# Kernel optimization log

Hardware: AMD Instinct MI355X
Metric: run time of the kernel (lower is better)

The kernel has to match this reference:

```python
import jax, jax.numpy as jnp
import numpy as np

N, K, D_IN, D_OUT = 50000, 16, 256, 256
LN_EPS = 1e-5


def setup_inputs() -> dict:
    key = jax.random.key(0)
    k1, k2, k3, k4 = jax.random.split(key, 4)
    features = jax.random.normal(k1, (N, D_IN), dtype=jnp.float32)
    neighbors = jax.random.randint(k2, (N, K), 0, N, dtype=jnp.int64)
    importance_weights = jax.random.uniform(k3, (N, K), dtype=jnp.float32)
    # Linear(in_channels, out_channels): weight stored as [D_IN, D_OUT] for x @ W + b
    W = jax.random.normal(k4, (D_IN, D_OUT), dtype=jnp.float32) * (1.0 / np.sqrt(D_IN))
    b = jnp.zeros((D_OUT,), dtype=jnp.float32)
    gamma = jnp.ones((D_OUT,), dtype=jnp.float32)
    beta = jnp.zeros((D_OUT,), dtype=jnp.float32)
    return {"features": features, "neighbors": neighbors,
            "importance_weights": importance_weights,
            "W": W, "b": b, "gamma": gamma, "beta": beta}


def reference(features, neighbors, importance_weights, W, b, gamma, beta):
    # Gather neighbor features: [N, K, D_IN]
    neigh_feats = features[neighbors]
    # Linear transform: [N, K, D_OUT]
    transformed = jnp.einsum('nkd,df->nkf', neigh_feats, W) + b
    # Normalize importance weights per node; zero-sum fallback = uniform mean
    wsum = jnp.sum(importance_weights, axis=-1, keepdims=True)  # [N, 1]
    norm_w = jnp.where(wsum == 0.0,
                       jnp.full_like(importance_weights, 1.0 / K),
                       importance_weights / jnp.where(wsum == 0.0, 1.0, wsum))
    # Importance-weighted sum over neighbors: [N, D_OUT]
    agg = jnp.einsum('nkf,nk->nf', transformed, norm_w)
    # LayerNorm over feature dim (torch: biased variance, eps=1e-5)
    mean = jnp.mean(agg, axis=-1, keepdims=True)
    var = jnp.mean((agg - mean) ** 2, axis=-1, keepdims=True)
    out = (agg - mean) * jax.lax.rsqrt(var + LN_EPS) * gamma + beta
    return out
```

## Files before the change

### kernel.cpp

```cpp
#include <hip/hip_runtime.h>


#define NN   50000
#define KNB  16
#define D    256
#define WSTR 272

typedef __attribute__((ext_vector_type(8))) short short8;
typedef __attribute__((ext_vector_type(4))) float f32x4;

static __device__ __forceinline__ unsigned short f2bf(float x) {
    unsigned int u = __float_as_uint(x);
    return (unsigned short)((u + 0x7FFFu + ((u >> 16) & 1u)) >> 16);
}
static __device__ __forceinline__ float bf2f(unsigned short h) {
    return __uint_as_float((unsigned int)h << 16);
}

__global__ __launch_bounds__(256) void convert_all(const float* __restrict__ feat,
                                                   const float* __restrict__ Wm,
                                                   unsigned short* __restrict__ featb,
                                                   unsigned short* __restrict__ wtp,
                                                   int nfb) {
    if ((int)blockIdx.x < nfb) {
        const size_t g = (size_t)blockIdx.x * 256 + threadIdx.x;
        const float4 a = *(const float4*)(feat + g * 8);
        const float4 b = *(const float4*)(feat + g * 8 + 4);
        short8 o;
        o[0] = (short)f2bf(a.x); o[1] = (short)f2bf(a.y);
        o[2] = (short)f2bf(a.z); o[3] = (short)f2bf(a.w);
        o[4] = (short)f2bf(b.x); o[5] = (short)f2bf(b.y);
        o[6] = (short)f2bf(b.z); o[7] = (short)f2bf(b.w);
        *(short8*)(featb + g * 8) = o;
    } else {
        const int g    = (blockIdx.x - nfb) * 256 + threadIdx.x;
        const int lane = g & 63;
        const int c    = (g >> 6) & 15;
        const int kb   = g >> 10;
        const int n    = c * 16 + (lane & 15);
        const int k0   = kb * 32 + (lane >> 4) * 8;
        short8 v;
        #pragma unroll
        for (int j = 0; j < 8; ++j) v[j] = (short)f2bf(Wm[(size_t)(k0 + j) * D + n]);
        *(short8*)(wtp + (size_t)g * 8) = v;
    }
}

__global__ __launch_bounds__(256, 8) void pool_b(const unsigned short* __restrict__ featb,
                                                 const int*   __restrict__ nbr,
                                                 const float* __restrict__ iw,
                                                 unsigned short* __restrict__ aggb) {
    const int  t    = threadIdx.x;
    const int  lane = t & 63;
    const int  wq   = t >> 6;
    const long n    = (long)blockIdx.x * 4 + wq;

    float ws = 0.f;
    #pragma unroll
    for (int k = 0; k < KNB; ++k) ws += iw[n * KNB + k];
    const bool  zs  = (ws == 0.f);
    const float inv = zs ? (1.f / KNB) : (1.f / ws);

    float4 p = make_float4(0.f, 0.f, 0.f, 0.f);
    #pragma unroll 1
    for (int kb = 0; kb < KNB; kb += 8) {
        int   idx[8];
        float w[8];
        #pragma unroll
        for (int k = 0; k < 8; ++k) {
            idx[k] = nbr[n * KNB + kb + k];
            w[k]   = iw [n * KNB + kb + k];
        }
        #pragma unroll
        for (int k = 0; k < 8; ++k) {
            const float   wk = zs ? inv : (w[k] * inv);
            const ushort4 u  = *(const ushort4*)(featb + (size_t)idx[k] * D + lane * 4);
            p.x += wk * bf2f(u.x); p.y += wk * bf2f(u.y);
            p.z += wk * bf2f(u.z); p.w += wk * bf2f(u.w);
        }
    }
    ushort4 o;
    o.x = f2bf(p.x); o.y = f2bf(p.y); o.z = f2bf(p.z); o.w = f2bf(p.w);
    *(ushort4*)(aggb + (size_t)n * 512 + lane * 4) = o;
}

__global__ __launch_bounds__(256, 8) void pool_f(const float* __restrict__ feat,
                                                 const int*   __restrict__ nbr,
                                                 const float* __restrict__ iw,
                                                 unsigned short* __restrict__ aggb) {
    const int  t    = threadIdx.x;
    const int  lane = t & 63;
    const int  wq   = t >> 6;
    const long n    = (long)blockIdx.x * 4 + wq;
    float ws = 0.f;
    #pragma unroll
    for (int k = 0; k < KNB; ++k) ws += iw[n * KNB + k];
    const bool  zs  = (ws == 0.f);
    const float inv = zs ? (1.f / KNB) : (1.f / ws);
    float4 p = make_float4(0.f, 0.f, 0.f, 0.f);
    #pragma unroll 1
    for (int kb = 0; kb < KNB; kb += 8) {
        int idx[8]; float w[8];
        #pragma unroll
        for (int k = 0; k < 8; ++k) { idx[k] = nbr[n*KNB+kb+k]; w[k] = iw[n*KNB+kb+k]; }
        #pragma unroll
        for (int k = 0; k < 8; ++k) {
            const float  wk = zs ? inv : (w[k] * inv);
            const float4 f  = *(const float4*)(feat + (size_t)idx[k] * D + lane * 4);
            p.x += wk*f.x; p.y += wk*f.y; p.z += wk*f.z; p.w += wk*f.w;
        }
    }
    ushort4 o;
    o.x = f2bf(p.x); o.y = f2bf(p.y); o.z = f2bf(p.z); o.w = f2bf(p.w);
    *(ushort4*)(aggb + (size_t)n * 512 + lane * 4) = o;
}

__global__ __launch_bounds__(256) void gemm_ln(const unsigned short* __restrict__ aggb,
                                               const unsigned short* __restrict__ wtp,
                                               const float* __restrict__ bias,
                                               const float* __restrict__ gamma,
                                               const float* __restrict__ beta,
                                               float* __restrict__ out) {
    __shared__ short sB[2][8192];
    __shared__ float fsh[4][4 * WSTR];

    const int t       = threadIdx.x;
    const int lane    = t & 63;
    const int wq      = t >> 6;
    const int quad    = lane >> 4;
    const int l15     = lane & 15;
    const int rowbase = blockIdx.x * 64 + wq * 16;

    const int arow = min(rowbase + l15, NN - 1);
    const unsigned short* aptr = aggb + (size_t)arow * 512 + quad * 8;
    const short8* wv = (const short8*)wtp;

    short8 aF[8];
    #pragma unroll
    for (int kb = 0; kb < 8; ++kb) aF[kb] = *(const short8*)(aptr + kb * 32);

    #pragma unroll
    for (int i = 0; i < 4; ++i)
        *(short8*)&sB[0][(size_t)(i * 256 + t) * 8] = wv[i * 256 + t];
    __syncthreads();

    f32x4 acc[16];
    #pragma unroll
    for (int c = 0; c < 16; ++c) acc[c] = (f32x4){0.f, 0.f, 0.f, 0.f};

    #pragma unroll
    for (int kb = 0; kb < 8; ++kb) {
        const int buf = kb & 1;
        short8 stg[4];
        if (kb < 7) {
            #pragma unroll
            for (int i = 0; i < 4; ++i)
                stg[i] = wv[(size_t)(kb + 1) * 1024 + i * 256 + t];
        }
        #pragma unroll
        for (int c = 0; c < 16; ++c) {
            const short8 b = *(const short8*)&sB[buf][(size_t)(c * 64 + lane) * 8];
            acc[c] = __builtin_amdgcn_mfma_f32_16x16x32_bf16(aF[kb], b, acc[c], 0, 0, 0);
        }
        if (kb < 7) {
            #pragma unroll
            for (int i = 0; i < 4; ++i)
                *(short8*)&sB[buf ^ 1][(size_t)(i * 256 + t) * 8] = stg[i];
        }
        __syncthreads();
    }

    float bv[16];
    #pragma unroll
    for (int c = 0; c < 16; ++c) bv[c] = bias[c * 16 + l15];
    const float4 gv4 = *(const float4*)(gamma + lane * 4);
    const float4 bt4 = *(const float4*)(beta  + lane * 4);
    float* wsh = fsh[wq];

    #pragma unroll
    for (int j = 0; j < 4; ++j) {
        float s = 0.f, sq = 0.f;
        #pragma unroll
        for (int c = 0; c < 16; ++c) {
            const float v = acc[c][j] + bv[c];
            s += v; sq += v * v;
        }
        #pragma unroll
        for (int off = 1; off < 16; off <<= 1) {
            s  += __shfl_xor(s,  off, 64);
            sq += __shfl_xor(sq, off, 64);
        }
        const float mean = s * (1.f / D);
        const float var  = sq * (1.f / D) - mean * mean;
        const float rstd = rsqrtf(var + 1e-5f);
        #pragma unroll
        for (int c = 0; c < 16; ++c)
            wsh[quad * WSTR + c * 16 + l15] = (acc[c][j] + bv[c] - mean) * rstd;
        #pragma unroll
        for (int p = 0; p < 4; ++p) {
            const long  r  = rowbase + p * 4 + j;
            if (r < NN) {
                const float4 v = *(const float4*)(wsh + p * WSTR + lane * 4);
                float4 o;
                o.x = v.x * gv4.x + bt4.x; o.y = v.y * gv4.y + bt4.y;
                o.z = v.z * gv4.z + bt4.z; o.w = v.w * gv4.w + bt4.w;
                *(float4*)(out + r * D + lane * 4) = o;
            }
        }
    }
}

extern "C" void kernel_launch(void* const* d_in, const int* in_sizes, int n_in,
                              void* d_out, int out_size, void* d_ws, size_t ws_size,
                              hipStream_t stream) {
    const float* feat = (const float*)d_in[0];
    const int*   nbr  = (const int*)d_in[1];
    const float* iw   = (const float*)d_in[2];
    const float* Wm   = (const float*)d_in[3];
    const float* b    = (const float*)d_in[4];
    const float* g    = (const float*)d_in[5];
    const float* be   = (const float*)d_in[6];
    float*       out  = (float*)d_out;

    unsigned short* wtp   = (unsigned short*)d_ws;
    unsigned short* featb = (unsigned short*)((char*)d_ws + 131072);
    unsigned short* aggb  = (unsigned short*)d_out;

    const size_t need = 131072 + (size_t)NN * D * 2;

    if (ws_size >= need) {
        convert_all<<<dim3(6282),   dim3(256), 0, stream>>>(feat, Wm, featb, wtp, 6250);
        pool_b     <<<dim3(NN / 4), dim3(256), 0, stream>>>(featb, nbr, iw, aggb);
    } else {
        convert_all<<<dim3(32),     dim3(256), 0, stream>>>(feat, Wm, featb, wtp, 0);
        pool_f     <<<dim3(NN / 4), dim3(256), 0, stream>>>(feat, nbr, iw, aggb);
    }
    gemm_ln<<<dim3((NN + 63) / 64), dim3(256), 0, stream>>>(aggb, wtp, b, g, be, out);
}
```

Before: 186.5 us.

## Split pooling into feature-dimension slices with neighbor-parallel lanes and shuffle reduction

Replaces the per-node pooling kernel with one where each block handles one 32-wide feature slice for 32 nodes. Within a wave, 8 lane groups each gather a different pair of neighbors, and the partial sums are combined with cross-lane shuffles. The slicing is meant to keep each block's gathers within a narrow column band for better cache locality, and to raise memory-level parallelism per node. Index and weight loads and the output store use nontemporal hints. In exchange, it adds shuffle-reduction work, each gather is only 8 bytes per lane, and every neighbor index is re-read once per slice.

```diff
diff --git a/kernel.cpp b/kernel.cpp
--- a/kernel.cpp
+++ b/kernel.cpp
@@ -5,9 +5,11 @@
 #define KNB  16
 #define D    256
 #define WSTR 272
+#define NPB  32
 
 typedef __attribute__((ext_vector_type(8))) short short8;
 typedef __attribute__((ext_vector_type(4))) float f32x4;
+typedef __attribute__((ext_vector_type(4))) unsigned short us4;
 
 static __device__ __forceinline__ unsigned short f2bf(float x) {
     unsigned int u = __float_as_uint(x);
@@ -46,42 +48,59 @@
     }
 }
 
-__global__ __launch_bounds__(256, 8) void pool_b(const unsigned short* __restrict__ featb,
-                                                 const int*   __restrict__ nbr,
-                                                 const float* __restrict__ iw,
-                                                 unsigned short* __restrict__ aggb) {
-    const int  t    = threadIdx.x;
-    const int  lane = t & 63;
-    const int  wq   = t >> 6;
-    const long n    = (long)blockIdx.x * 4 + wq;
-
-    float ws = 0.f;
-    #pragma unroll
-    for (int k = 0; k < KNB; ++k) ws += iw[n * KNB + k];
-    const bool  zs  = (ws == 0.f);
-    const float inv = zs ? (1.f / KNB) : (1.f / ws);
-
-    float4 p = make_float4(0.f, 0.f, 0.f, 0.f);
+__global__ __launch_bounds__(256, 8) void pool_slices(
+        const unsigned short* __restrict__ featb,
+        const int*   __restrict__ nbr,
+        const float* __restrict__ iw,
+        unsigned short* __restrict__ aggb) {
+    const int t     = threadIdx.x;
+    const int lane  = t & 63;
+    const int wq    = t >> 6;
+    const int s     = blockIdx.x & 7;
+    const int chunk = blockIdx.x >> 3;
+    const int dl    = lane & 7;
+    const int kg    = lane >> 3;
+    const int dbase = s * 32 + dl * 4;
+
+    const int n0 = chunk * NPB + wq * (NPB / 4);
     #pragma unroll 1
-    for (int kb = 0; kb < KNB; kb += 8) {
-        int   idx[8];
-        float w[8];
-        #pragma unroll
-        for (int k = 0; k < 8; ++k) {
-            idx[k] = nbr[n * KNB + kb + k];
-            w[k]   = iw [n * KNB + kb + k];
-        }
-        #pragma unroll
-        for (int k = 0; k < 8; ++k) {
-            const float   wk = zs ? inv : (w[k] * inv);
-            const ushort4 u  = *(const ushort4*)(featb + (size_t)idx[k] * D + lane * 4);
-            p.x += wk * bf2f(u.x); p.y += wk * bf2f(u.y);
-            p.z += wk * bf2f(u.z); p.w += wk * bf2f(u.w);
-        }
-    }
-    ushort4 o;
-    o.x = f2bf(p.x); o.y = f2bf(p.y); o.z = f2bf(p.z); o.w = f2bf(p.w);
-    *(ushort4*)(aggb + (size_t)n * 512 + lane * 4) = o;
+    for (int j = 0; j < NPB / 4; ++j) {
+        const int n = n0 + j;
+        if (n >= NN) break;
+        const size_t base = (size_t)n * KNB;
+        const int   i0 = __builtin_nontemporal_load(nbr + base + kg);
+        const int   i1 = __builtin_nontemporal_load(nbr + base + 8 + kg);
+        const float w0 = __builtin_nontemporal_load(iw  + base + kg);
+        const float w1 = __builtin_nontemporal_load(iw  + base + 8 + kg);
+        float ws = w0 + w1;
+        ws += __shfl_xor(ws, 8,  64);
+        ws += __shfl_xor(ws, 16, 64);
+        ws += __shfl_xor(ws, 32, 64);
+        const bool  zsum = (ws == 0.f);
+        const float inv  = zsum ? (1.f / KNB) : (1.f / ws);
+        const float f0   = zsum ? inv : (w0 * inv);
+        const float f1   = zsum ? inv : (w1 * inv);
+        const us4 u0 = *(const us4*)(featb + (size_t)i0 * D + dbase);
+        const us4 u1 = *(const us4*)(featb + (size_t)i1 * D + dbase);
+        float4 p;
+        p.x = f0 * bf2f(u0[0]) + f1 * bf2f(u1[0]);
+        p.y = f0 * bf2f(u0[1]) + f1 * bf2f(u1[1]);
+        p.z = f0 * bf2f(u0[2]) + f1 * bf2f(u1[2]);
+        p.w = f0 * bf2f(u0[3]) + f1 * bf2f(u1[3]);
+        #pragma unroll
+        for (int off = 8; off < 64; off <<= 1) {
+            p.x += __shfl_xor(p.x, off, 64);
+            p.y += __shfl_xor(p.y, off, 64);
+            p.z += __shfl_xor(p.z, off, 64);
+            p.w += __shfl_xor(p.w, off, 64);
+        }
+        if (kg == 0) {
+            us4 o;
+            o[0] = f2bf(p.x); o[1] = f2bf(p.y); o[2] = f2bf(p.z); o[3] = f2bf(p.w);
+            __builtin_nontemporal_store(o,
+                (us4*)(aggb + (size_t)n * 512 + dbase));
+        }
+    }
 }
 
 __global__ __launch_bounds__(256, 8) void pool_f(const float* __restrict__ feat,
@@ -229,10 +248,11 @@
     const size_t need = 131072 + (size_t)NN * D * 2;
 
     if (ws_size >= need) {
-        convert_all<<<dim3(6282),   dim3(256), 0, stream>>>(feat, Wm, featb, wtp, 6250);
-        pool_b     <<<dim3(NN / 4), dim3(256), 0, stream>>>(featb, nbr, iw, aggb);
+        convert_all<<<dim3(6282), dim3(256), 0, stream>>>(feat, Wm, featb, wtp, 6250);
+        pool_slices<<<dim3(8 * ((NN + NPB - 1) / NPB)), dim3(256), 0, stream>>>(
+            featb, nbr, iw, aggb);
     } else {
-        convert_all<<<dim3(32),     dim3(256), 0, stream>>>(feat, Wm, featb, wtp, 0);
+        convert_all<<<dim3(32),   dim3(256), 0, stream>>>(feat, Wm, aggb, wtp, 0);
         pool_f     <<<dim3(NN / 4), dim3(256), 0, stream>>>(feat, nbr, iw, aggb);
     }
     gemm_ln<<<dim3((NN + 63) / 64), dim3(256), 0, stream>>>(aggb, wtp, b, g, be, out);
```

Result: slower. 233.4 us (+25.2%).

## Store bf16 features slice-major and gather per 32-column slice for cache locality

Applied to the files above, without the earlier changes.

The bf16 conversion now writes features in a slice-major layout, with 8 slices of 32 columns each. A new pool kernel assigns each block one slice and 32 nodes, so the random neighbor gathers only touch a 3.2MB slice that can stay resident in L2/LLC. Neighbor indices and weights are loaded cooperatively and broadcast with shuffles, and the aggregate goes to a separate workspace buffer with a 256-element stride. The cost is smaller 8-byte gathers per lane, an extra workspace requirement, and the risk that falling back to the old path changes behaviour when the workspace is too small.

```diff
diff --git a/kernel.cpp b/kernel.cpp
--- a/kernel.cpp
+++ b/kernel.cpp
@@ -8,6 +8,9 @@
 
 typedef __attribute__((ext_vector_type(8))) short short8;
 typedef __attribute__((ext_vector_type(4))) float f32x4;
+typedef __attribute__((ext_vector_type(4))) unsigned short us4;
+typedef __attribute__((ext_vector_type(2))) int   i32x2;
+typedef __attribute__((ext_vector_type(2))) float f32x2;
 
 static __device__ __forceinline__ unsigned short f2bf(float x) {
     unsigned int u = __float_as_uint(x);
@@ -21,7 +24,7 @@
                                                    const float* __restrict__ Wm,
                                                    unsigned short* __restrict__ featb,
                                                    unsigned short* __restrict__ wtp,
-                                                   int nfb) {
+                                                   int nfb, int slicemaj) {
     if ((int)blockIdx.x < nfb) {
         const size_t g = (size_t)blockIdx.x * 256 + threadIdx.x;
         const float4 a = *(const float4*)(feat + g * 8);
@@ -31,7 +34,15 @@
         o[2] = (short)f2bf(a.z); o[3] = (short)f2bf(a.w);
         o[4] = (short)f2bf(b.x); o[5] = (short)f2bf(b.y);
         o[6] = (short)f2bf(b.z); o[7] = (short)f2bf(b.w);
-        *(short8*)(featb + g * 8) = o;
+        if (slicemaj) {
+            const int n  = (int)(g >> 5);
+            const int s  = ((int)g >> 2) & 7;
+            const int d0 = ((int)g & 3) * 8;
+            *(short8*)(featb + (size_t)s * ((size_t)NN * 32)
+                             + (size_t)n * 32 + d0) = o;
+        } else {
+            *(short8*)(featb + g * 8) = o;
+        }
     } else {
         const int g    = (blockIdx.x - nfb) * 256 + threadIdx.x;
         const int lane = g & 63;
@@ -46,10 +57,63 @@
     }
 }
 
+__global__ __launch_bounds__(256) void pool_sg(
+        const unsigned short* __restrict__ featb,
+        const int*   __restrict__ nbr,
+        const float* __restrict__ iw,
+        unsigned short* __restrict__ aggb, int astr) {
+    const int t     = threadIdx.x;
+    const int lane  = t & 63;
+    const int wq    = t >> 6;
+    const int s     = blockIdx.x & 7;
+    const int chunk = blockIdx.x >> 3;
+    const int nd    = lane >> 3;
+    const int dl    = lane & 7;
+    const int n     = chunk * 32 + wq * 8 + nd;
+    const int nc    = min(n, NN - 1);
+    const unsigned short* fs = featb + (size_t)s * ((size_t)NN * 32);
+
+    const i32x2 i2 = __builtin_nontemporal_load(
+        (const i32x2*)(nbr + (size_t)nc * KNB + dl * 2));
+    const f32x2 w2 = __builtin_nontemporal_load(
+        (const f32x2*)(iw  + (size_t)nc * KNB + dl * 2));
+
+    float ws = w2[0] + w2[1];
+    ws += __shfl_xor(ws, 1, 64);
+    ws += __shfl_xor(ws, 2, 64);
+    ws += __shfl_xor(ws, 4, 64);
+    const bool  zs  = (ws == 0.f);
+    const float inv = zs ? (1.f / KNB) : (1.f / ws);
+    f32x2 wn;
+    wn[0] = zs ? inv : w2[0] * inv;
+    wn[1] = zs ? inv : w2[1] * inv;
+
+    float4 p = make_float4(0.f, 0.f, 0.f, 0.f);
+    const int sbase = nd * 8;
+    #pragma unroll
+    for (int k = 0; k < KNB; ++k) {
+        const int   src = sbase + (k >> 1);
+        const int   ik  = __shfl((k & 1) ? i2[1] : i2[0], src, 64);
+        const float wk  = __shfl((k & 1) ? wn[1] : wn[0], src, 64);
+        const us4   u   = *(const us4*)(fs + (size_t)(unsigned)ik * 32 + dl * 4);
+        p.x += wk * bf2f(u[0]);
+        p.y += wk * bf2f(u[1]);
+        p.z += wk * bf2f(u[2]);
+        p.w += wk * bf2f(u[3]);
+    }
+    if (n < NN) {
+        us4 o;
+        o[0] = f2bf(p.x); o[1] = f2bf(p.y); o[2] = f2bf(p.z); o[3] = f2bf(p.w);
+        __builtin_nontemporal_store(o,
+            (us4*)(aggb + (size_t)n * astr + s * 32 + dl * 4));
+    }
+}
+
 __global__ __launch_bounds__(256, 8) void pool_b(const unsigned short* __restrict__ featb,
                                                  const int*   __restrict__ nbr,
                                                  const float* __restrict__ iw,
-                                                 unsigned short* __restrict__ aggb) {
+                                                 unsigned short* __restrict__ aggb,
+                                                 int astr) {
     const int  t    = threadIdx.x;
     const int  lane = t & 63;
     const int  wq   = t >> 6;
@@ -81,13 +145,14 @@
     }
     ushort4 o;
     o.x = f2bf(p.x); o.y = f2bf(p.y); o.z = f2bf(p.z); o.w = f2bf(p.w);
-    *(ushort4*)(aggb + (size_t)n * 512 + lane * 4) = o;
+    *(ushort4*)(aggb + (size_t)n * astr + lane * 4) = o;
 }
 
 __global__ __launch_bounds__(256, 8) void pool_f(const float* __restrict__ feat,
                                                  const int*   __restrict__ nbr,
                                                  const float* __restrict__ iw,
-                                                 unsigned short* __restrict__ aggb) {
+                                                 unsigned short* __restrict__ aggb,
+                                                 int astr) {
     const int  t    = threadIdx.x;
     const int  lane = t & 63;
     const int  wq   = t >> 6;
@@ -112,10 +177,11 @@
     }
     ushort4 o;
     o.x = f2bf(p.x); o.y = f2bf(p.y); o.z = f2bf(p.z); o.w = f2bf(p.w);
-    *(ushort4*)(aggb + (size_t)n * 512 + lane * 4) = o;
+    *(ushort4*)(aggb + (size_t)n * astr + lane * 4) = o;
 }
 
 __global__ __launch_bounds__(256) void gemm_ln(const unsigned short* __restrict__ aggb,
+                                               int astr,
                                                const unsigned short* __restrict__ wtp,
                                                const float* __restrict__ bias,
                                                const float* __restrict__ gamma,
@@ -132,7 +198,7 @@
     const int rowbase = blockIdx.x * 64 + wq * 16;
 
     const int arow = min(rowbase + l15, NN - 1);
-    const unsigned short* aptr = aggb + (size_t)arow * 512 + quad * 8;
+    const unsigned short* aptr = aggb + (size_t)arow * astr + quad * 8;
     const short8* wv = (const short8*)wtp;
 
     short8 aF[8];
@@ -222,18 +288,30 @@
     const float* be   = (const float*)d_in[6];
     float*       out  = (float*)d_out;
 
-    unsigned short* wtp   = (unsigned short*)d_ws;
-    unsigned short* featb = (unsigned short*)((char*)d_ws + 131072);
-    unsigned short* aggb  = (unsigned short*)d_out;
-
-    const size_t need = 131072 + (size_t)NN * D * 2;
-
-    if (ws_size >= need) {
-        convert_all<<<dim3(6282),   dim3(256), 0, stream>>>(feat, Wm, featb, wtp, 6250);
-        pool_b     <<<dim3(NN / 4), dim3(256), 0, stream>>>(featb, nbr, iw, aggb);
+    const size_t featB = (size_t)NN * D * 2;
+    unsigned short* wtp    = (unsigned short*)d_ws;
+    unsigned short* featb  = (unsigned short*)((char*)d_ws + 131072);
+    unsigned short* aggb_w = (unsigned short*)((char*)d_ws + 131072 + featB);
+
+    if (ws_size >= 131072 + 2 * featB) {
+        convert_all<<<dim3(6282), dim3(256), 0, stream>>>(feat, Wm, featb, wtp,
+                                                          6250, 1);
+        pool_sg<<<dim3(8 * ((NN + 31) / 32)), dim3(256), 0, stream>>>(
+            featb, nbr, iw, aggb_w, 256);
+        gemm_ln<<<dim3((NN + 63) / 64), dim3(256), 0, stream>>>(
+            aggb_w, 256, wtp, b, g, be, out);
+    } else if (ws_size >= 131072 + featB) {
+        unsigned short* aggb = (unsigned short*)d_out;
+        convert_all<<<dim3(6282), dim3(256), 0, stream>>>(feat, Wm, featb, wtp,
+                                                          6250, 0);
+        pool_b<<<dim3(NN / 4), dim3(256), 0, stream>>>(featb, nbr, iw, aggb, 512);
+        gemm_ln<<<dim3((NN + 63) / 64), dim3(256), 0, stream>>>(
+            aggb, 512, wtp, b, g, be, out);
     } else {
-        convert_all<<<dim3(32),     dim3(256), 0, stream>>>(feat, Wm, featb, wtp, 0);
-        pool_f     <<<dim3(NN / 4), dim3(256), 0, stream>>>(feat, nbr, iw, aggb);
-    }
-    gemm_ln<<<dim3((NN + 63) / 64), dim3(256), 0, stream>>>(aggb, wtp, b, g, be, out);
-}
+        unsigned short* aggb = (unsigned short*)d_out;
+        convert_all<<<dim3(32), dim3(256), 0, stream>>>(feat, Wm, featb, wtp, 0, 0);
+        pool_f<<<dim3(NN / 4), dim3(256), 0, stream>>>(feat, nbr, iw, aggb, 512);
+        gemm_ln<<<dim3((NN + 63) / 64), dim3(256), 0, stream>>>(
+            aggb, 512, wtp, b, g, be, out);
+    }
+}
```

New measurement: 191.3 us. 1.03x slower.

## Add persistent GEMM+LayerNorm kernel with full weight tile resident in LDS

Applied to the files above, without the earlier changes.

Adds a persistent gemm_lnr kernel launched with 256 blocks of 6 waves. Each block loads the whole bf16 weight matrix (128 KB) into LDS once, then loops over 16-row tiles, so the weight is not restaged per 64-row block. When workspace allows, the pooled aggregate is written to a separate compact buffer (stride 256) instead of aliasing the output with stride 512. The large LDS footprint limits occupancy to one block per CU, and the grid of 256 persistent blocks may underfill or imbalance the device.

```diff
diff --git a/kernel.cpp b/kernel.cpp
--- a/kernel.cpp
+++ b/kernel.cpp
@@ -5,6 +5,7 @@
 #define KNB  16
 #define D    256
 #define WSTR 272
+#define GWAVES 6
 
 typedef __attribute__((ext_vector_type(8))) short short8;
 typedef __attribute__((ext_vector_type(4))) float f32x4;
@@ -49,7 +50,8 @@
 __global__ __launch_bounds__(256, 8) void pool_b(const unsigned short* __restrict__ featb,
                                                  const int*   __restrict__ nbr,
                                                  const float* __restrict__ iw,
-                                                 unsigned short* __restrict__ aggb) {
+                                                 unsigned short* __restrict__ aggb,
+                                                 int astr) {
     const int  t    = threadIdx.x;
     const int  lane = t & 63;
     const int  wq   = t >> 6;
@@ -81,13 +83,14 @@
     }
     ushort4 o;
     o.x = f2bf(p.x); o.y = f2bf(p.y); o.z = f2bf(p.z); o.w = f2bf(p.w);
-    *(ushort4*)(aggb + (size_t)n * 512 + lane * 4) = o;
+    *(ushort4*)(aggb + (size_t)n * astr + lane * 4) = o;
 }
 
 __global__ __launch_bounds__(256, 8) void pool_f(const float* __restrict__ feat,
                                                  const int*   __restrict__ nbr,
                                                  const float* __restrict__ iw,
-                                                 unsigned short* __restrict__ aggb) {
+                                                 unsigned short* __restrict__ aggb,
+                                                 int astr) {
     const int  t    = threadIdx.x;
     const int  lane = t & 63;
     const int  wq   = t >> 6;
@@ -112,10 +115,97 @@
     }
     ushort4 o;
     o.x = f2bf(p.x); o.y = f2bf(p.y); o.z = f2bf(p.z); o.w = f2bf(p.w);
-    *(ushort4*)(aggb + (size_t)n * 512 + lane * 4) = o;
+    *(ushort4*)(aggb + (size_t)n * astr + lane * 4) = o;
+}
+
+__global__ __launch_bounds__(384) void gemm_lnr(const unsigned short* __restrict__ aggb,
+                                                int astr,
+                                                const unsigned short* __restrict__ wtp,
+                                                const float* __restrict__ bias,
+                                                const float* __restrict__ gamma,
+                                                const float* __restrict__ beta,
+                                                float* __restrict__ out) {
+    __shared__ short sB[65536];
+    __shared__ float fsh[GWAVES][4 * WSTR];
+
+    const int t    = threadIdx.x;
+    const int lane = t & 63;
+    const int w    = t >> 6;
+    const int quad = lane >> 4;
+    const int l15  = lane & 15;
+
+    const short8* wv  = (const short8*)wtp;
+    short8*       sB8 = (short8*)sB;
+    for (int u = t; u < 8192; u += 384) sB8[u] = wv[u];
+    __syncthreads();
+
+    float bv[16];
+    #pragma unroll
+    for (int c = 0; c < 16; ++c) bv[c] = bias[c * 16 + l15];
+    const float4 gv4 = *(const float4*)(gamma + lane * 4);
+    const float4 bt4 = *(const float4*)(beta  + lane * 4);
+    float* wsh = fsh[w];
+
+    const int NT = (NN + 15) / 16;
+    for (int tile = blockIdx.x * GWAVES + w; tile < NT; tile += 256 * GWAVES) {
+        const int rowbase = tile * 16;
+        const int arow    = min(rowbase + l15, NN - 1);
+        const unsigned short* aptr = aggb + (size_t)arow * astr + quad * 8;
+
+        short8 aF[8];
+        #pragma unroll
+        for (int kb = 0; kb < 8; ++kb) aF[kb] = *(const short8*)(aptr + kb * 32);
+
+        f32x4 acc[16];
+        #pragma unroll
+        for (int c = 0; c < 16; ++c) acc[c] = (f32x4){0.f, 0.f, 0.f, 0.f};
+
+        #pragma unroll
+        for (int kb = 0; kb < 8; ++kb) {
+            #pragma unroll
+            for (int c = 0; c < 16; ++c) {
+                const short8 b = sB8[kb * 1024 + c * 64 + lane];
+                acc[c] = __builtin_amdgcn_mfma_f32_16x16x32_bf16(aF[kb], b, acc[c],
+                                                                 0, 0, 0);
+            }
+        }
+
+        #pragma unroll
+        for (int j = 0; j < 4; ++j) {
+            float s = 0.f, sq = 0.f;
+            #pragma unroll
+            for (int c = 0; c < 16; ++c) {
+                const float v = acc[c][j] + bv[c];
+                s += v; sq += v * v;
+            }
+            #pragma unroll
+            for (int off = 1; off < 16; off <<= 1) {
+                s  += __shfl_xor(s,  off, 64);
+                sq += __shfl_xor(sq, off, 64);
+            }
+            const float mean = s * (1.f / D);
+            const float var  = sq * (1.f / D) - mean * mean;
+            const float rstd = rsqrtf(var + 1e-5f);
+            #pragma unroll
+            for (int c = 0; c < 16; ++c)
+                wsh[quad * WSTR + c * 16 + l15] = (acc[c][j] + bv[c] - mean) * rstd;
+            #pragma unroll
+            for (int p = 0; p < 4; ++p) {
+                const long r = rowbase + p * 4 + j;
+                if (r < NN) {
+                    const float4 v = *(const float4*)(wsh + p * WSTR + lane * 4);
+                    float4 o;
+                    o.x = v.x * gv4.x + bt4.x; o.y = v.y * gv4.y + bt4.y;
+                    o.z = v.z * gv4.z + bt4.z; o.w = v.w * gv4.w + bt4.w;
+                    *(float4*)(out + r * D + lane * 4) = o;
+                }
+            }
+        }
+    }
 }
 
 __global__ __launch_bounds__(256) void gemm_ln(const unsigned short* __restrict__ aggb,
+                                               int astr,
                                                const unsigned short* __restrict__ wtp,
                                                const float* __restrict__ bias,
                                                const float* __restrict__ gamma,
@@ -132,7 +222,7 @@
     const int rowbase = blockIdx.x * 64 + wq * 16;
 
     const int arow = min(rowbase + l15, NN - 1);
-    const unsigned short* aptr = aggb + (size_t)arow * 512 + quad * 8;
+    const unsigned short* aptr = aggb + (size_t)arow * astr + quad * 8;
     const short8* wv = (const short8*)wtp;
 
     short8 aF[8];
@@ -198,7 +288,7 @@
             wsh[quad * WSTR + c * 16 + l15] = (acc[c][j] + bv[c] - mean) * rstd;
         #pragma unroll
         for (int p = 0; p < 4; ++p) {
-            const long  r  = rowbase + p * 4 + j;
+            const long r = rowbase + p * 4 + j;
             if (r < NN) {
                 const float4 v = *(const float4*)(wsh + p * WSTR + lane * 4);
                 float4 o;
@@ -222,18 +312,26 @@
     const float* be   = (const float*)d_in[6];
     float*       out  = (float*)d_out;
 
-    unsigned short* wtp   = (unsigned short*)d_ws;
-    unsigned short* featb = (unsigned short*)((char*)d_ws + 131072);
-    unsigned short* aggb  = (unsigned short*)d_out;
-
-    const size_t need = 131072 + (size_t)NN * D * 2;
-
-    if (ws_size >= need) {
-        convert_all<<<dim3(6282),   dim3(256), 0, stream>>>(feat, Wm, featb, wtp, 6250);
-        pool_b     <<<dim3(NN / 4), dim3(256), 0, stream>>>(featb, nbr, iw, aggb);
+    const size_t featB = (size_t)NN * D * 2;
+    unsigned short* wtp    = (unsigned short*)d_ws;
+    unsigned short* featb  = (unsigned short*)((char*)d_ws + 131072);
+    unsigned short* aggb_w = (unsigned short*)((char*)d_ws + 131072 + featB);
+
+    if (ws_size >= 131072 + 2 * featB) {
+        convert_all<<<dim3(6282), dim3(256), 0, stream>>>(feat, Wm, featb, wtp, 6250);
+        pool_b<<<dim3(NN / 4), dim3(256), 0, stream>>>(featb, nbr, iw, aggb_w, 256);
+        gemm_lnr<<<dim3(256), dim3(384), 0, stream>>>(aggb_w, 256, wtp, b, g, be, out);
+    } else if (ws_size >= 131072 + featB) {
+        unsigned short* aggb = (unsigned short*)d_out;
+        convert_all<<<dim3(6282), dim3(256), 0, stream>>>(feat, Wm, featb, wtp, 6250);
+        pool_b<<<dim3(NN / 4), dim3(256), 0, stream>>>(featb, nbr, iw, aggb, 512);
+        gemm_ln<<<dim3((NN + 63) / 64), dim3(256), 0, stream>>>(
+            aggb, 512, wtp, b, g, be, out);
     } else {
-        convert_all<<<dim3(32),     dim3(256), 0, stream>>>(feat, Wm, featb, wtp, 0);
-        pool_f     <<<dim3(NN / 4), dim3(256), 0, stream>>>(feat, nbr, iw, aggb);
-    }
-    gemm_ln<<<dim3((NN + 63) / 64), dim3(256), 0, stream>>>(aggb, wtp, b, g, be, out);
-}
+        unsigned short* aggb = (unsigned short*)d_out;
+        convert_all<<<dim3(32), dim3(256), 0, stream>>>(feat, Wm, featb, wtp, 0);
+        pool_f<<<dim3(NN / 4), dim3(256), 0, stream>>>(feat, nbr, iw, aggb, 512);
+        gemm_ln<<<dim3((NN + 63) / 64), dim3(256), 0, stream>>>(
+            aggb, 512, wtp, b, g, be, out);
+    }
+}
```

Result: slower. 318.2 us (+70.6%).
